# Performance work log

Hardware: AMD Instinct MI355X
Metric: run time of the kernel (lower is better)

Reference implementation:

```python
import jax, jax.numpy as jnp
import numpy as np

B, N, C = 16, 1024, 256
SIZE = (512, 640)          # (H, W) image size
STRIDE = 8
H0, W0 = SIZE[0] // STRIDE, SIZE[1] // STRIDE   # 64, 80
P_TOK = H0 * W0                                  # 5120 base tokens
NHEAD, NLVL, NPTS = 8, 4, 4
HD = C // NHEAD
NUM_CLASSES = 7


def setup_inputs() -> dict:
    key = jax.random.key(0)
    ks = jax.random.split(key, 16)
    g = lambda k, shape, s=0.02: jax.random.normal(k, shape, jnp.float32) * s
    return {
        "q_t": jax.random.normal(ks[0], (B, N, C), jnp.float32),
        "h_t": jax.random.normal(ks[1], (B, P_TOK, C), jnp.float32),
        "p_head_t": jax.random.uniform(ks[2], (B, N, 2), jnp.float32)
                    * jnp.array([SIZE[1], SIZE[0]], jnp.float32),  # (x,y) in image coords
        "W_off": g(ks[3], (C, NHEAD * NLVL * NPTS * 2)),
        "b_off": g(ks[4], (NHEAD * NLVL * NPTS * 2,)),
        "W_attn": g(ks[5], (C, NHEAD * NLVL * NPTS)),
        "b_attn": g(ks[6], (NHEAD * NLVL * NPTS,)),
        "W_v": g(ks[7], (C, C)), "b_v": g(ks[8], (C,)),
        "W_o": g(ks[9], (C, C)), "b_o": g(ks[10], (C,)),
        "W_p1": g(ks[11], (2 * C, C)), "b_p1": g(ks[12], (C,)),
        "W_p2": g(ks[13], (C, NUM_CLASSES)), "b_p2": g(ks[14], (NUM_CLASSES,)),
    }


def _bilinear_sample(value_l, loc):
    """value_l: (B,Hl,Wl,nh,hd); loc: (B,N,nh,NPTS,2) in [0,1] normalized (x,y).
    grid_sample semantics: align_corners=False, padding_mode='zeros'.
    Returns (B,nh,N,NPTS,hd)."""
    Bb, Hl, Wl = value_l.shape[0], value_l.shape[1], value_l.shape[2]
    x = loc[..., 0] * Wl - 0.5
    y = loc[..., 1] * Hl - 0.5
    x0 = jnp.floor(x); y0 = jnp.floor(y)
    wx = x - x0; wy = y - y0
    x0i = x0.astype(jnp.int32); y0i = y0.astype(jnp.int32)
    flat = value_l.reshape(Bb, Hl * Wl, NHEAD, HD).transpose(0, 2, 1, 3)  # (B,nh,S,hd)

    def corner(xi, yi):
        valid = ((xi >= 0) & (xi < Wl) & (yi >= 0) & (yi < Hl)).astype(value_l.dtype)
        idx = (jnp.clip(yi, 0, Hl - 1) * Wl + jnp.clip(xi, 0, Wl - 1)).transpose(0, 2, 1, 3)  # (B,nh,N,P)
        g = jnp.take_along_axis(flat, idx.reshape(Bb, NHEAD, -1)[..., None], axis=2)
        g = g.reshape(Bb, NHEAD, idx.shape[2], idx.shape[3], HD)
        return g * valid.transpose(0, 2, 1, 3)[..., None]

    tw = lambda w: w.transpose(0, 2, 1, 3)[..., None]  # (B,nh,N,P,1)
    return (corner(x0i, y0i) * tw((1 - wx) * (1 - wy))
            + corner(x0i + 1, y0i) * tw(wx * (1 - wy))
            + corner(x0i, y0i + 1) * tw((1 - wx) * wy)
            + corner(x0i + 1, y0i + 1) * tw(wx * wy))


def reference(q_t, h_t, p_head_t, W_off, b_off, W_attn, b_attn,
              W_v, b_v, W_o, b_o, W_p1, b_p1, W_p2, b_p2):
    # normalize point predictions to [0,1] (x by W, y by H)
    p_norm = jnp.clip(p_head_t / jnp.array([SIZE[1], SIZE[0]], jnp.float32), 0.0, 1.0)

    # ---- get_deformable_inputs: 4-level pyramid by 2x2 average pooling ----
    cur = h_t.reshape(B, H0, W0, C)
    feats, shapes = [], []
    for l in range(NLVL):
        feats.append(cur)
        shapes.append((cur.shape[1], cur.shape[2]))
        if l < NLVL - 1:
            h, w = cur.shape[1], cur.shape[2]
            cur = cur.reshape(B, h // 2, 2, w // 2, 2, C).mean(axis=(2, 4))
    f_scales = jnp.concatenate([f.reshape(B, -1, C) for f in feats], axis=1)  # (B,S,C)

    # ---- DMSMHA_Block (multi-scale deformable attention) ----
    value = (f_scales @ W_v + b_v).reshape(B, -1, NHEAD, HD)
    offsets = (q_t @ W_off + b_off).reshape(B, N, NHEAD, NLVL, NPTS, 2)
    attn = jax.nn.softmax(
        (q_t @ W_attn + b_attn).reshape(B, N, NHEAD, NLVL * NPTS), axis=-1
    ).reshape(B, N, NHEAD, NLVL, NPTS)

    out = jnp.zeros((B, NHEAD, N, HD), jnp.float32)
    start = 0
    for l, (Hl, Wl) in enumerate(shapes):
        Sl = Hl * Wl
        vl = value[:, start:start + Sl].reshape(B, Hl, Wl, NHEAD, HD)
        start += Sl
        norm = jnp.array([Wl, Hl], jnp.float32)
        loc = p_norm[:, :, None, None, :] + offsets[:, :, :, l] / norm  # (B,N,nh,P,2)
        sampled = _bilinear_sample(vl, loc)                              # (B,nh,N,P,hd)
        w = attn[:, :, :, l].transpose(0, 2, 1, 3)                       # (B,nh,N,P)
        out = out + jnp.einsum('bhnp,bhnpd->bhnd', w, sampled)

    q_local = out.transpose(0, 2, 1, 3).reshape(B, N, C) @ W_o + b_o

    # ---- fuse + MLP head ----
    q_fused = jnp.concatenate([q_t, q_local], axis=-1)
    hid = jax.nn.relu(q_fused @ W_p1 + b_p1)
    logits = hid @ W_p2 + b_p2   # (B,N,num_classes)
    return logits
```

## Files before the change

kernel.cpp:

```cpp
#include <hip/hip_runtime.h>
#include <math.h>


namespace {

constexpr int kB = 16;
constexpr int kN = 1024;
constexpr int kC = 256;
constexpr int kNCLS = 7;
constexpr int kSTOT = 6800;

typedef __attribute__((ext_vector_type(8))) short short8;
typedef __attribute__((ext_vector_type(4))) float f32x4;

__device__ inline ushort f2bf(float f) {
  union { float f; unsigned u; } v; v.f = f;
  unsigned r = (v.u + 0x7fffu + ((v.u >> 16) & 1u)) >> 16;
  return (ushort)r;
}
__device__ inline float bf2f(ushort h) {
  union { unsigned u; float f; } v; v.u = ((unsigned)h) << 16;
  return v.f;
}

__device__ inline void gload16(const ushort* g, ushort* l) {
  __builtin_amdgcn_global_load_lds(
      (const __attribute__((address_space(1))) void*)g,
      (__attribute__((address_space(3))) void*)l, 16, 0, 0);
}

__global__ void cast_f2b_kernel(const float* __restrict__ in, ushort* __restrict__ out, int n4) {
  int i = blockIdx.x * 256 + threadIdx.x;
  if (i >= n4) return;
  float4 v = ((const float4*)in)[i];
  ((ushort4*)out)[i] = make_ushort4(f2bf(v.x), f2bf(v.y), f2bf(v.z), f2bf(v.w));
}

__global__ void pool_b2b_kernel(const ushort* __restrict__ fin, ushort* __restrict__ fout,
                                int oh, int ow, int so_in, int so_out) {
  int idx = blockIdx.x * 256 + threadIdx.x;
  if (idx >= kB * oh * ow * kC) return;
  int c = idx & 255; int t = idx >> 8;
  int x = t % ow; t /= ow; int y = t % oh; int b = t / oh;
  int iw = ow * 2;
  const ushort* p = fin + (((size_t)b * kSTOT + so_in + y * 2 * iw + x * 2) << 8) + c;
  float s = 0.25f * (bf2f(p[0]) + bf2f(p[256]) + bf2f(p[iw * 256]) + bf2f(p[iw * 256 + 256]));
  fout[(((size_t)b * kSTOT + so_out + y * ow + x) << 8) + c] = f2bf(s);
}

__global__ void wtrans_all_kernel(const float* __restrict__ s0, const float* __restrict__ s1,
                                  const float* __restrict__ s2, const float* __restrict__ s3,
                                  const float* __restrict__ s4,
                                  ushort* __restrict__ d0, ushort* __restrict__ d1,
                                  ushort* __restrict__ d2, ushort* __restrict__ d3,
                                  ushort* __restrict__ d4) {
  __shared__ float t[32][33];
  const float* W; ushort* Wt; int K, N;
  switch (blockIdx.z) {
    case 0: W = s0; Wt = d0; K = 256; N = 256; break;
    case 1: W = s1; Wt = d1; K = 256; N = 256; break;
    case 2: W = s2; Wt = d2; K = 256; N = 128; break;
    case 3: W = s3; Wt = d3; K = 256; N = 256; break;
    default: W = s4; Wt = d4; K = 512; N = 256; break;
  }
  int nx = blockIdx.x << 5, ky = blockIdx.y << 5;
  if (nx >= N || ky >= K) return;
  int lx = threadIdx.x & 31, ly = threadIdx.x >> 5;
#pragma unroll
  for (int i = 0; i < 32; i += 8)
    t[ly + i][lx] = W[(size_t)(ky + ly + i) * N + nx + lx];
  __syncthreads();
#pragma unroll
  for (int i = 0; i < 32; i += 8)
    Wt[(size_t)(nx + ly + i) * K + ky + lx] = f2bf(t[lx][ly + i]);
}

__global__ void wcomb_kernel(const float* __restrict__ W_o, const float* __restrict__ W_p1,
                             const float* __restrict__ b_o, const float* __restrict__ b_p1,
                             const ushort* __restrict__ Wt_p1,
                             ushort* __restrict__ Wt_p1c, float* __restrict__ bp1c) {
  __shared__ float wcol[256];
  __shared__ float wsum[4];
  int h = blockIdx.x;
  int in = threadIdx.x;
  wcol[in] = W_p1[(size_t)(256 + in) * 256 + h];
  __syncthreads();
  float s = 0.f;
  const float* wo = W_o + (size_t)in * 256;
#pragma unroll 4
  for (int out = 0; out < 256; ++out) s = fmaf(wo[out], wcol[out], s);
  Wt_p1c[(size_t)h * 512 + 256 + in] = f2bf(s);
  Wt_p1c[(size_t)h * 512 + in] = Wt_p1[(size_t)h * 512 + in];
  float part = b_o[in] * wcol[in];
#pragma unroll
  for (int m = 32; m > 0; m >>= 1) part += __shfl_xor(part, m);
  if ((in & 63) == 0) wsum[in >> 6] = part;
  __syncthreads();
  if (in == 0) bp1c[h] = b_p1[h] + wsum[0] + wsum[1] + wsum[2] + wsum[3];
}

template <int KTOT, bool SPLITK, int OMODE, bool RELU>
__global__ __launch_bounds__(256) void gemm_bf16_kernel(
    const ushort* __restrict__ A, const ushort* __restrict__ A2,
    const ushort* __restrict__ Wt, const float* __restrict__ bias,
    const float* __restrict__ bias2, void* __restrict__ Cout,
    void* __restrict__ Cout2, int ldc) {
  __shared__ ushort Asm[2][128 * 32];
  __shared__ ushort Bsm[2][128 * 32];
  const int tid = threadIdx.x;
  const int w = tid >> 6, l = tid & 63;
  const int bm = blockIdx.y << 7, bn = blockIdx.x << 7;
  const int wm = w >> 1, wn = w & 1;

  const int c0 = w * 2, c1 = w * 2 + 1;
  const int G0 = c0 * 64 + l, G1 = c1 * 64 + l;
  const int r0 = G0 >> 2, g0 = G0 & 3;
  const int r1 = G1 >> 2, g1 = G1 & 3;
  const int sz0 = (g0 ^ ((r0 >> 1) & 3)) << 3;
  const int sz1 = (g1 ^ ((r1 >> 1) & 3)) << 3;
  const int ak = SPLITK ? 256 : KTOT;
  const ushort* sA0 = A + (size_t)(bm + r0) * ak + sz0;
  const ushort* sA1 = A + (size_t)(bm + r1) * ak + sz1;
  const ushort* sA0b = SPLITK ? A2 + (size_t)(bm + r0) * 256 + sz0 : nullptr;
  const ushort* sA1b = SPLITK ? A2 + (size_t)(bm + r1) * 256 + sz1 : nullptr;
  const ushort* sB0 = Wt + (size_t)(bn + r0) * KTOT + sz0;
  const ushort* sB1 = Wt + (size_t)(bn + r1) * KTOT + sz1;

  const int e = l >> 4, rl = l & 15;
  int aoff[4], boff[4];
#pragma unroll
  for (int i = 0; i < 4; ++i) {
    int r = wm * 64 + i * 16 + rl;
    aoff[i] = r * 32 + ((e ^ ((r >> 1) & 3)) << 3);
    int rb = wn * 64 + i * 16 + rl;
    boff[i] = rb * 32 + ((e ^ ((rb >> 1) & 3)) << 3);
  }

  f32x4 acc[4][4];
#pragma unroll
  for (int i = 0; i < 4; ++i)
#pragma unroll
    for (int j = 0; j < 4; ++j) acc[i][j] = (f32x4){0.f, 0.f, 0.f, 0.f};

  auto stage = [&](int buf, int k0) {
    const ushort *a0, *a1;
    if (SPLITK && k0 >= 256) {
      a0 = sA0b + (k0 - 256);
      a1 = sA1b + (k0 - 256);
    } else {
      a0 = sA0 + k0;
      a1 = sA1 + k0;
    }
    gload16(a0, &Asm[buf][c0 * 512]);
    gload16(a1, &Asm[buf][c1 * 512]);
    gload16(sB0 + k0, &Bsm[buf][c0 * 512]);
    gload16(sB1 + k0, &Bsm[buf][c1 * 512]);
  };

  constexpr int nt = KTOT / 32;
  stage(0, 0);
  __syncthreads();
  for (int t = 0; t < nt; ++t) {
    const int cur = t & 1;
    if (t + 1 < nt) stage(cur ^ 1, (t + 1) * 32);
    short8 af[4], bfr[4];
#pragma unroll
    for (int i = 0; i < 4; ++i) af[i] = *(const short8*)&Asm[cur][aoff[i]];
#pragma unroll
    for (int j = 0; j < 4; ++j) bfr[j] = *(const short8*)&Bsm[cur][boff[j]];
#pragma unroll
    for (int i = 0; i < 4; ++i)
#pragma unroll
      for (int j = 0; j < 4; ++j)
        acc[i][j] = __builtin_amdgcn_mfma_f32_16x16x32_bf16(bfr[j], af[i], acc[i][j], 0, 0, 0);
    __syncthreads();
  }

#pragma unroll
  for (int j = 0; j < 4; ++j) {
    int ch = bn + wn * 64 + j * 16 + e * 4;
    float4 b4;
    if (OMODE == 2)
      b4 = (ch < 256) ? *(const float4*)(bias + ch) : *(const float4*)(bias2 + ch - 256);
    else
      b4 = *(const float4*)(bias + ch);
    float bv[4] = {b4.x, b4.y, b4.z, b4.w};
#pragma unroll
    for (int i = 0; i < 4; ++i) {
      int sp = bm + wm * 64 + i * 16 + rl;
      float v[4];
#pragma unroll
      for (int r = 0; r < 4; ++r) {
        v[r] = acc[i][j][r] + bv[r];
        if (RELU) v[r] = fmaxf(v[r], 0.f);
      }
      if (OMODE == 0) {
        *(float4*)&((float*)Cout)[(size_t)sp * ldc + ch] = make_float4(v[0], v[1], v[2], v[3]);
      } else if (OMODE == 1) {
        *(ushort4*)&((ushort*)Cout)[(size_t)sp * ldc + ch] =
            make_ushort4(f2bf(v[0]), f2bf(v[1]), f2bf(v[2]), f2bf(v[3]));
      } else {
        if (ch < 256)
          *(float4*)&((float*)Cout)[(size_t)sp * 256 + ch] = make_float4(v[0], v[1], v[2], v[3]);
        else
          *(float4*)&((float*)Cout2)[(size_t)sp * 128 + (ch - 256)] =
              make_float4(v[0], v[1], v[2], v[3]);
      }
    }
  }
}

__global__ __launch_bounds__(256) void gemm_f32a_kernel(
    const float* __restrict__ A, const ushort* __restrict__ Wt,
    const float* __restrict__ bias, ushort* __restrict__ Cout) {
  __shared__ ushort Asm[2][128 * 32];
  __shared__ ushort Bsm[2][128 * 32];
  const int tid = threadIdx.x;
  const int w = tid >> 6, l = tid & 63;
  const int by = blockIdx.y;
  const int bn = blockIdx.x << 7;
  const int bm = by << 7;
  const int wm = w >> 1, wn = w & 1;

  const int ar = tid >> 1, ah = tid & 1;
  const float* aSrc = A + (size_t)(bm + ar) * 256 + ah * 16;
  const int s_ar = (ar >> 1) & 3;
  const int ad0 = ar * 32 + (((2 * ah + 0) ^ s_ar) << 3);
  const int ad1 = ar * 32 + (((2 * ah + 1) ^ s_ar) << 3);

  const int c0 = w * 2, c1 = w * 2 + 1;
  const int G0 = c0 * 64 + l, G1 = c1 * 64 + l;
  const int r0 = G0 >> 2, g0 = G0 & 3;
  const int r1 = G1 >> 2, g1 = G1 & 3;
  const ushort* sB0 = Wt + (size_t)(bn + r0) * 256 + ((g0 ^ ((r0 >> 1) & 3)) << 3);
  const ushort* sB1 = Wt + (size_t)(bn + r1) * 256 + ((g1 ^ ((r1 >> 1) & 3)) << 3);

  const int e = l >> 4, rl = l & 15;
  int aoff[4], boff[4];
#pragma unroll
  for (int i = 0; i < 4; ++i) {
    int r = wm * 64 + i * 16 + rl;
    aoff[i] = r * 32 + ((e ^ ((r >> 1) & 3)) << 3);
    int rb = wn * 64 + i * 16 + rl;
    boff[i] = rb * 32 + ((e ^ ((rb >> 1) & 3)) << 3);
  }

  f32x4 acc[4][4];
#pragma unroll
  for (int i = 0; i < 4; ++i)
#pragma unroll
    for (int j = 0; j < 4; ++j) acc[i][j] = (f32x4){0.f, 0.f, 0.f, 0.f};

  float4 av[4];
  auto loadA = [&](int k0) {
#pragma unroll
    for (int q = 0; q < 4; ++q) av[q] = *(const float4*)(aSrc + k0 + 4 * q);
  };
  auto writeA = [&](int buf) {
    ushort u[16];
#pragma unroll
    for (int q = 0; q < 4; ++q) {
      u[4 * q + 0] = f2bf(av[q].x);
      u[4 * q + 1] = f2bf(av[q].y);
      u[4 * q + 2] = f2bf(av[q].z);
      u[4 * q + 3] = f2bf(av[q].w);
    }
    *(short8*)&Asm[buf][ad0] =
        (short8){(short)u[0], (short)u[1], (short)u[2], (short)u[3],
                 (short)u[4], (short)u[5], (short)u[6], (short)u[7]};
    *(short8*)&Asm[buf][ad1] =
        (short8){(short)u[8], (short)u[9], (short)u[10], (short)u[11],
                 (short)u[12], (short)u[13], (short)u[14], (short)u[15]};
  };
  auto stageB = [&](int buf, int k0) {
    gload16(sB0 + k0, &Bsm[buf][c0 * 512]);
    gload16(sB1 + k0, &Bsm[buf][c1 * 512]);
  };

  loadA(0);
  stageB(0, 0);
  writeA(0);
  __syncthreads();
  for (int t = 0; t < 8; ++t) {
    const int cur = t & 1;
    if (t < 7) {
      loadA((t + 1) * 32);
      stageB(cur ^ 1, (t + 1) * 32);
    }
    short8 af[4], bfr[4];
#pragma unroll
    for (int i = 0; i < 4; ++i) af[i] = *(const short8*)&Asm[cur][aoff[i]];
#pragma unroll
    for (int j = 0; j < 4; ++j) bfr[j] = *(const short8*)&Bsm[cur][boff[j]];
#pragma unroll
    for (int i = 0; i < 4; ++i)
#pragma unroll
      for (int j = 0; j < 4; ++j)
        acc[i][j] = __builtin_amdgcn_mfma_f32_16x16x32_bf16(bfr[j], af[i], acc[i][j], 0, 0, 0);
    if (t < 7) writeA(cur ^ 1);
    __syncthreads();
  }

  const int b = by / 40;
  const int sb = (by - b * 40) << 7;
  ushort* outB = Cout + (((size_t)(b * 6800 + sb)) << 8);
#pragma unroll
  for (int j = 0; j < 4; ++j) {
    int ch = bn + wn * 64 + j * 16 + e * 4;
    float4 b4 = *(const float4*)(bias + ch);
    float bv[4] = {b4.x, b4.y, b4.z, b4.w};
#pragma unroll
    for (int i = 0; i < 4; ++i) {
      int sp = wm * 64 + i * 16 + rl;
      float v[4];
#pragma unroll
      for (int r = 0; r < 4; ++r) v[r] = acc[i][j][r] + bv[r];
      *(ushort4*)&outB[(size_t)sp * 256 + ch] =
          make_ushort4(f2bf(v[0]), f2bf(v[1]), f2bf(v[2]), f2bf(v[3]));
    }
  }
}

__global__ void deform_kernel(
    const ushort* __restrict__ value, const float* __restrict__ off,
    const float* __restrict__ attnl, const float* __restrict__ p_head,
    ushort* __restrict__ samp) {
  int blk = (int)blockIdx.x;
  int sw = (blk & 7) * 256 + (blk >> 3);
  int wvi = (sw << 2) + (threadIdx.x >> 6);
  int l = threadIdx.x & 63;
  int nq = l >> 5;
  int lh = l & 31;
  int h = lh >> 2;
  int pt = wvi * 2 + nq;
  int b = pt >> 10;
  size_t bn = (size_t)pt;

  float ph = (lh < 2) ? p_head[bn * 2 + lh] : 0.f;
  float px = __shfl(ph, (nq << 5) + 0, 64) * (1.0f / 640.0f);
  float py = __shfl(ph, (nq << 5) + 1, 64) * (1.0f / 512.0f);
  px = fminf(fmaxf(px, 0.f), 1.f);
  py = fminf(fmaxf(py, 0.f), 1.f);

  const float4* offp = (const float4*)(off + (bn << 8));
  float4 ofv0 = offp[2 * lh];
  float4 ofv1 = offp[2 * lh + 1];
  float4 atv = ((const float4*)(attnl + (bn << 7)))[lh];

  float m = fmaxf(fmaxf(atv.x, atv.y), fmaxf(atv.z, atv.w));
  m = fmaxf(m, __shfl_xor(m, 1, 64));
  m = fmaxf(m, __shfl_xor(m, 2, 64));
  float e0 = expf(atv.x - m), e1 = expf(atv.y - m);
  float e2 = expf(atv.z - m), e3 = expf(atv.w - m);
  float s = e0 + e1 + e2 + e3;
  s += __shfl_xor(s, 1, 64);
  s += __shfl_xor(s, 2, 64);
  float inv = 1.f / s;
  atv = make_float4(e0 * inv, e1 * inv, e2 * inv, e3 * inv);

  float acc[8];
#pragma unroll
  for (int i = 0; i < 8; ++i) acc[i] = 0.f;
  const ushort* vbb = value + (((size_t)b * kSTOT) << 8) + (lh << 3);

#pragma unroll 1
  for (int lv = 0; lv < 4; ++lv) {
    const int Wl = 80 >> lv, Hl = 64 >> lv;
    const int offL = (lv == 0) ? 0 : (lv == 1) ? 5120 : (lv == 2) ? 6400 : 6720;
    const ushort* vb = vbb + (((size_t)offL) << 8);
    const int src = (nq << 5) + (h << 2) + lv;
    const float fx = px * (float)Wl - 0.5f;
    const float fy = py * (float)Hl - 0.5f;
#pragma unroll
    for (int pp = 0; pp < 4; ++pp) {
      float sx, sy;
      if ((pp >> 1) == 0) {
        sx = (pp & 1) ? ofv0.z : ofv0.x;
        sy = (pp & 1) ? ofv0.w : ofv0.y;
      } else {
        sx = (pp & 1) ? ofv1.z : ofv1.x;
        sy = (pp & 1) ? ofv1.w : ofv1.y;
      }
      float ox = __shfl(sx, src, 64);
      float oy = __shfl(sy, src, 64);
      float sa = pp == 0 ? atv.x : pp == 1 ? atv.y : pp == 2 ? atv.z : atv.w;
      float aw = __shfl(sa, src, 64);

      float xx = fx + ox;
      float yy = fy + oy;
      float x0f = floorf(xx), y0f = floorf(yy);
      float wx = xx - x0f, wy = yy - y0f;
      int x0 = (int)x0f, y0 = (int)y0f;
      float w00 = (1.f - wx) * (1.f - wy) * aw;
      float w01 = wx * (1.f - wy) * aw;
      float w10 = (1.f - wx) * wy * aw;
      float w11 = wx * wy * aw;
      auto corner = [&](int xi, int yi, float wgt) {
        bool valid = (xi >= 0) && (xi < Wl) && (yi >= 0) && (yi < Hl);
        int xc = xi < 0 ? 0 : (xi > Wl - 1 ? Wl - 1 : xi);
        int yc = yi < 0 ? 0 : (yi > Hl - 1 ? Hl - 1 : yi);
        short8 d = *(const short8*)(vb + (((size_t)(yc * Wl + xc)) << 8));
        float wg = valid ? wgt : 0.f;
#pragma unroll
        for (int i = 0; i < 8; ++i) acc[i] = fmaf(wg, bf2f((ushort)d[i]), acc[i]);
      };
      corner(x0, y0, w00);
      corner(x0 + 1, y0, w01);
      corner(x0, y0 + 1, w10);
      corner(x0 + 1, y0 + 1, w11);
    }
  }
  ushort o[8];
#pragma unroll
  for (int i = 0; i < 8; ++i) o[i] = f2bf(acc[i]);
  *(short8*)(samp + (bn << 8) + (lh << 3)) =
      (short8){(short)o[0], (short)o[1], (short)o[2], (short)o[3],
               (short)o[4], (short)o[5], (short)o[6], (short)o[7]};
}

__global__ void head_kernel(const float* __restrict__ hid, const float* __restrict__ W2,
                            const float* __restrict__ b2, float* __restrict__ outp) {
  int gid = blockIdx.x * 256 + threadIdx.x;
  int wave = gid >> 6;
  int lane = threadIdx.x & 63;
  if (wave >= kB * kN) return;
  const float* hrow = hid + ((size_t)wave << 8);
  float acc[kNCLS];
#pragma unroll
  for (int j = 0; j < kNCLS; ++j) acc[j] = 0.f;
  for (int k = lane; k < kC; k += 64) {
    float hv = hrow[k];
    const float* wr = W2 + k * kNCLS;
#pragma unroll
    for (int j = 0; j < kNCLS; ++j) acc[j] = fmaf(hv, wr[j], acc[j]);
  }
#pragma unroll
  for (int m = 32; m > 0; m >>= 1) {
#pragma unroll
    for (int j = 0; j < kNCLS; ++j) acc[j] += __shfl_xor(acc[j], m);
  }
  float r = 0.f;
#pragma unroll
  for (int j = 0; j < kNCLS; ++j)
    if (lane == j) r = acc[j] + b2[j];
  if (lane < kNCLS) outp[(size_t)wave * kNCLS + lane] = r;
}

}

extern "C" void kernel_launch(void* const* d_in, const int* in_sizes, int n_in,
                              void* d_out, int out_size, void* d_ws, size_t ws_size,
                              hipStream_t stream) {
  const float* q_t    = (const float*)d_in[0];
  const float* h_t    = (const float*)d_in[1];
  const float* p_head = (const float*)d_in[2];
  const float* W_off  = (const float*)d_in[3];
  const float* b_off  = (const float*)d_in[4];
  const float* W_attn = (const float*)d_in[5];
  const float* b_attn = (const float*)d_in[6];
  const float* W_v    = (const float*)d_in[7];
  const float* b_v    = (const float*)d_in[8];
  const float* W_o    = (const float*)d_in[9];
  const float* b_o    = (const float*)d_in[10];
  const float* W_p1   = (const float*)d_in[11];
  const float* b_p1   = (const float*)d_in[12];
  const float* W_p2   = (const float*)d_in[13];
  const float* b_p2   = (const float*)d_in[14];
  float* out = (float*)d_out;
  char* wsb = (char*)d_ws;

  ushort* value = (ushort*)(wsb + 55705600);
  ushort* q_bf  = (ushort*)(wsb + 111411200);
  float*  offb  = (float*)(wsb + 119799808);
  float*  attnl = (float*)(wsb + 136577024);
  ushort* samp  = (ushort*)(wsb + 144965632);
  float*  hid   = (float*)(wsb + 161742848);
  ushort* wtp   = (ushort*)(wsb + 178520064);
  ushort* Wt_v   = wtp;
  ushort* Wt_oa  = wtp + 65536;
  ushort* Wt_o   = wtp + 163840;
  ushort* Wt_p1  = wtp + 229376;
  ushort* Wt_p1c = wtp + 360448;
  float*  bp1c   = (float*)(wtp + 491520);

  cast_f2b_kernel<<<4096, 256, 0, stream>>>(q_t, q_bf, kB * kN * 64);

  wtrans_all_kernel<<<dim3(8, 16, 5), 256, 0, stream>>>(
      W_v, W_off, W_attn, W_o, W_p1,
      Wt_v, Wt_oa, Wt_oa + 65536, Wt_o, Wt_p1);

  wcomb_kernel<<<256, 256, 0, stream>>>(W_o, W_p1, b_o, b_p1, Wt_p1, Wt_p1c, bp1c);

  gemm_f32a_kernel<<<dim3(2, 640), 256, 0, stream>>>(h_t, Wt_v, b_v, value);

  pool_b2b_kernel<<<20480, 256, 0, stream>>>(value, value, 32, 40, 0, 5120);
  pool_b2b_kernel<<<5120, 256, 0, stream>>>(value, value, 16, 20, 5120, 6400);
  pool_b2b_kernel<<<1280, 256, 0, stream>>>(value, value, 8, 10, 6400, 6720);

  gemm_bf16_kernel<256, false, 2, false><<<dim3(3, 128), 256, 0, stream>>>(
      q_bf, nullptr, Wt_oa, b_off, b_attn, offb, attnl, 256);

  deform_kernel<<<2048, 256, 0, stream>>>(value, offb, attnl, p_head, samp);

  gemm_bf16_kernel<512, true, 0, true><<<dim3(2, 128), 256, 0, stream>>>(
      q_bf, samp, Wt_p1c, bp1c, nullptr, hid, nullptr, 256);

  head_kernel<<<4096, 256, 0, stream>>>(hid, W_p2, b_p2, out);
}
```

Baseline: 155.2 us.

## Fuse three pyramid pooling launches into one kernel and single-buffer value GEMM

Replaces the three per-level 2x2 average-pool launches with one kernel. Each block reads an 8x8 patch of the base level once and writes levels 1-3 from registers, which removes the re-reads of the intermediate levels and two launches. Separately, the value-projection GEMM drops LDS double buffering in favour of a single buffer with two barriers per k-step. This halves its LDS footprint, which may raise occupancy, but it exposes load latency. Level 2/3 values are now computed from fp32 intermediates instead of bf16-rounded ones, so rounding changes slightly.

```diff
diff --git a/kernel.cpp b/kernel.cpp
--- a/kernel.cpp
+++ b/kernel.cpp
@@ -36,16 +36,37 @@
   ((ushort4*)out)[i] = make_ushort4(f2bf(v.x), f2bf(v.y), f2bf(v.z), f2bf(v.w));
 }
 
-__global__ void pool_b2b_kernel(const ushort* __restrict__ fin, ushort* __restrict__ fout,
-                                int oh, int ow, int so_in, int so_out) {
-  int idx = blockIdx.x * 256 + threadIdx.x;
-  if (idx >= kB * oh * ow * kC) return;
-  int c = idx & 255; int t = idx >> 8;
-  int x = t % ow; t /= ow; int y = t % oh; int b = t / oh;
-  int iw = ow * 2;
-  const ushort* p = fin + (((size_t)b * kSTOT + so_in + y * 2 * iw + x * 2) << 8) + c;
-  float s = 0.25f * (bf2f(p[0]) + bf2f(p[256]) + bf2f(p[iw * 256]) + bf2f(p[iw * 256 + 256]));
-  fout[(((size_t)b * kSTOT + so_out + y * ow + x) << 8) + c] = f2bf(s);
+__global__ void pool_all_kernel(ushort* __restrict__ val) {
+  int blk = blockIdx.x;
+  int X = blk % 10;
+  int t2 = blk / 10;
+  int Y = t2 % 8;
+  int b = t2 / 8;
+  int c = threadIdx.x;
+  const ushort* base = val + (((size_t)b * kSTOT + (Y * 8) * 80 + X * 8) << 8) + c;
+
+  float l1[16];
+#pragma unroll
+  for (int i = 0; i < 16; ++i) {
+    int iy = i >> 2, ix = i & 3;
+    const ushort* p = base + (((iy * 2) * 80 + ix * 2) << 8);
+    l1[i] = 0.25f * (bf2f(p[0]) + bf2f(p[256]) + bf2f(p[80 * 256]) + bf2f(p[80 * 256 + 256]));
+  }
+#pragma unroll
+  for (int i = 0; i < 16; ++i) {
+    int iy = i >> 2, ix = i & 3;
+    val[(((size_t)b * kSTOT + 5120 + (Y * 4 + iy) * 40 + X * 4 + ix) << 8) + c] = f2bf(l1[i]);
+  }
+  float l2[4];
+#pragma unroll
+  for (int j = 0; j < 4; ++j) {
+    int jy = j >> 1, jx = j & 1;
+    l2[j] = 0.25f * (l1[(2 * jy) * 4 + 2 * jx] + l1[(2 * jy) * 4 + 2 * jx + 1] +
+                     l1[(2 * jy + 1) * 4 + 2 * jx] + l1[(2 * jy + 1) * 4 + 2 * jx + 1]);
+    val[(((size_t)b * kSTOT + 6400 + (Y * 2 + jy) * 20 + X * 2 + jx) << 8) + c] = f2bf(l2[j]);
+  }
+  float l3 = 0.25f * (l2[0] + l2[1] + l2[2] + l2[3]);
+  val[(((size_t)b * kSTOT + 6720 + Y * 10 + X) << 8) + c] = f2bf(l3);
 }
 
 __global__ void wtrans_all_kernel(const float* __restrict__ s0, const float* __restrict__ s1,
@@ -213,8 +234,8 @@
 __global__ __launch_bounds__(256) void gemm_f32a_kernel(
     const float* __restrict__ A, const ushort* __restrict__ Wt,
     const float* __restrict__ bias, ushort* __restrict__ Cout) {
-  __shared__ ushort Asm[2][128 * 32];
-  __shared__ ushort Bsm[2][128 * 32];
+  __shared__ ushort Asm[128 * 32];
+  __shared__ ushort Bsm[128 * 32];
   const int tid = threadIdx.x;
   const int w = tid >> 6, l = tid & 63;
   const int by = blockIdx.y;
@@ -256,7 +277,7 @@
 #pragma unroll
     for (int q = 0; q < 4; ++q) av[q] = *(const float4*)(aSrc + k0 + 4 * q);
   };
-  auto writeA = [&](int buf) {
+  auto writeA = [&]() {
     ushort u[16];
 #pragma unroll
     for (int q = 0; q < 4; ++q) {
@@ -265,40 +286,33 @@
       u[4 * q + 2] = f2bf(av[q].z);
       u[4 * q + 3] = f2bf(av[q].w);
     }
-    *(short8*)&Asm[buf][ad0] =
-        (short8){(short)u[0], (short)u[1], (short)u[2], (short)u[3],
-                 (short)u[4], (short)u[5], (short)u[6], (short)u[7]};
-    *(short8*)&Asm[buf][ad1] =
-        (short8){(short)u[8], (short)u[9], (short)u[10], (short)u[11],
-                 (short)u[12], (short)u[13], (short)u[14], (short)u[15]};
+    *(short8*)&Asm[ad0] = (short8){(short)u[0], (short)u[1], (short)u[2], (short)u[3],
+                                   (short)u[4], (short)u[5], (short)u[6], (short)u[7]};
+    *(short8*)&Asm[ad1] = (short8){(short)u[8], (short)u[9], (short)u[10], (short)u[11],
+                                   (short)u[12], (short)u[13], (short)u[14], (short)u[15]};
   };
-  auto stageB = [&](int buf, int k0) {
-    gload16(sB0 + k0, &Bsm[buf][c0 * 512]);
-    gload16(sB1 + k0, &Bsm[buf][c1 * 512]);
+  auto stageB = [&](int k0) {
+    gload16(sB0 + k0, &Bsm[c0 * 512]);
+    gload16(sB1 + k0, &Bsm[c1 * 512]);
   };
 
   loadA(0);
-  stageB(0, 0);
-  writeA(0);
-  __syncthreads();
   for (int t = 0; t < 8; ++t) {
-    const int cur = t & 1;
-    if (t < 7) {
-      loadA((t + 1) * 32);
-      stageB(cur ^ 1, (t + 1) * 32);
-    }
+    if (t) __syncthreads();
+    writeA();
+    stageB(t * 32);
+    __syncthreads();
     short8 af[4], bfr[4];
 #pragma unroll
-    for (int i = 0; i < 4; ++i) af[i] = *(const short8*)&Asm[cur][aoff[i]];
-#pragma unroll
-    for (int j = 0; j < 4; ++j) bfr[j] = *(const short8*)&Bsm[cur][boff[j]];
+    for (int i = 0; i < 4; ++i) af[i] = *(const short8*)&Asm[aoff[i]];
+#pragma unroll
+    for (int j = 0; j < 4; ++j) bfr[j] = *(const short8*)&Bsm[boff[j]];
+    if (t < 7) loadA((t + 1) * 32);
 #pragma unroll
     for (int i = 0; i < 4; ++i)
 #pragma unroll
       for (int j = 0; j < 4; ++j)
         acc[i][j] = __builtin_amdgcn_mfma_f32_16x16x32_bf16(bfr[j], af[i], acc[i][j], 0, 0, 0);
-    if (t < 7) writeA(cur ^ 1);
-    __syncthreads();
   }
 
   const int b = by / 40;
@@ -493,9 +507,7 @@
 
   gemm_f32a_kernel<<<dim3(2, 640), 256, 0, stream>>>(h_t, Wt_v, b_v, value);
 
-  pool_b2b_kernel<<<20480, 256, 0, stream>>>(value, value, 32, 40, 0, 5120);
-  pool_b2b_kernel<<<5120, 256, 0, stream>>>(value, value, 16, 20, 5120, 6400);
-  pool_b2b_kernel<<<1280, 256, 0, stream>>>(value, value, 8, 10, 6400, 6720);
+  pool_all_kernel<<<1280, 256, 0, stream>>>(value);
 
   gemm_bf16_kernel<256, false, 2, false><<<dim3(3, 128), 256, 0, stream>>>(
       q_bf, nullptr, Wt_oa, b_off, b_attn, offb, attnl, 256);
```

After: 144.7 us. 6.7% less time.
